# Kernel optimization log

Hardware: AMD Instinct MI355X
Metric: run time of the kernel (lower is better)

Reference implementation:

```python
import jax, jax.numpy as jnp
import numpy as np

B = 10      # number of interacting objects
NDIM = 2    # self.n: position/velocity dimensionality

# Edge list equivalent to rel_rec/rel_send one-hot matrices (edges grouped by receiver)
_rec_idx, _send_idx = np.where(~np.eye(B, dtype=bool))


def _mlp(x, W0, b0, W1, b1, W2, b2):
    # MLP with 2 hidden softplus layers, linear output
    h = jax.nn.softplus(x @ W0 + b0)
    h = jax.nn.softplus(h @ W1 + b1)
    return h @ W2 + b2


def setup_inputs() -> dict:
    key = jax.random.key(0)
    ks = jax.random.split(key, 7)
    N = 8192            # trajectories per batch
    H = 128             # hidden width of self-dynamics MLP
    Hi = 128            # hidden width of interaction MLP
    nin = 2 * NDIM      # self MLP input dim (pos+vel)
    nout = 2 * NDIM     # n_f_out for order=1
    nin_i = 3 * NDIM    # interaction MLP input dim (p1-p2, v1, v2)
    w = lambda k, shp: jax.random.normal(k, shp, jnp.float32) / np.float32(np.sqrt(shp[0]))
    return {
        "z": jax.random.normal(ks[0], (N * B, 2 * NDIM), jnp.float32),
        "fW0": w(ks[1], (nin, H)),   "fb0": jnp.zeros((H,), jnp.float32),
        "fW1": w(ks[2], (H, H)),     "fb1": jnp.zeros((H,), jnp.float32),
        "fW2": w(ks[3], (H, nout)),  "fb2": jnp.zeros((nout,), jnp.float32),
        "iW0": w(ks[4], (nin_i, Hi)),"ib0": jnp.zeros((Hi,), jnp.float32),
        "iW1": w(ks[5], (Hi, Hi)),   "ib1": jnp.zeros((Hi,), jnp.float32),
        "iW2": w(ks[6], (Hi, nout)), "ib2": jnp.zeros((nout,), jnp.float32),
    }


def reference(z, fW0, fb0, fW1, fb1, fW2, fb2, iW0, ib0, iW1, ib1, iW2, ib2):
    # One evaluation of the ODE vector field (order=1, n_aug_dyn=n_aug_st=0).
    n = NDIM
    NB = z.shape[0]
    N = NB // B
    dz_self = _mlp(z, fW0, fb0, fW1, fb1, fW2, fb2)            # [N*B, 2n]
    z3 = z.reshape(N, B, 2 * n)
    recv = z3[:, _rec_idx]                                     # [N, B(B-1), 2n] gather (node2edge)
    send = z3[:, _send_idx]
    # odefint input: (p_recv - p_send, v_recv, v_send)  -> [N, B(B-1), 3n]
    inp = jnp.concatenate([recv[..., :n] - send[..., :n], recv[..., n:], send[..., n:]], -1)
    dz_int = _mlp(inp, iW0, ib0, iW1, ib1, iW2, ib2)           # [N, B(B-1), 2n]
    dz_int = dz_int.reshape(N, B, B - 1, 2 * n).sum(2)         # sum over senders per receiver
    dz = dz_self.reshape(N, B, 2 * n) + dz_int
    return dz.reshape(NB, 2 * n)
```

## Files before the change

kernel.cpp:

```cpp
#include <hip/hip_runtime.h>
#include <hip/hip_bf16.h>

#define NDIM 2
#define BB 10
#define H 128
#define PAIRS 90
#define ROWS 112
#define LDH 136
#define LOG2E 1.4426950408889634f
#define LN2   0.6931471805599453f

typedef short short8 __attribute__((ext_vector_type(8)));
typedef float floatx4 __attribute__((ext_vector_type(4)));

__device__ inline short f2bf(float x) {
    unsigned u = __float_as_uint(x);
    return (short)((u + 0x7fffu + ((u >> 16) & 1u)) >> 16);
}

#if __has_builtin(__builtin_amdgcn_cvt_pk_bf16_f32)
typedef __bf16 bf16x2_t __attribute__((ext_vector_type(2)));
__device__ inline unsigned pk2(float a, float b) {
    bf16x2_t v = __builtin_amdgcn_cvt_pk_bf16_f32(a, b);
    return __builtin_bit_cast(unsigned, v);
}
#else
__device__ inline unsigned pk2(float a, float b) {
    unsigned ua = __float_as_uint(a), ub = __float_as_uint(b);
    ua = (ua + 0x7fffu + ((ua >> 16) & 1u)) >> 16;
    ub = (ub + 0x7fffu + ((ub >> 16) & 1u)) & 0xffff0000u;
    return ua | ub;
}
#endif

__device__ inline float sp2(float xs) {
#if __has_builtin(__builtin_amdgcn_exp2f) && __has_builtin(__builtin_amdgcn_logf)
    float t = __builtin_amdgcn_exp2f(xs);
    return __builtin_amdgcn_logf(1.f + t) * LN2;
#else
    return log2f(1.f + exp2f(xs)) * LN2;
#endif
}

__global__ void prep_weights(const float* __restrict__ iW1, const float* __restrict__ fW1,
                             const float* __restrict__ iW2, const float* __restrict__ fW2,
                             const float* __restrict__ ib1, const float* __restrict__ fb1,
                             short* __restrict__ W1Fi, short* __restrict__ W1Ff,
                             short* __restrict__ W2Fi, short* __restrict__ W2Ff,
                             float* __restrict__ ib1s, float* __restrict__ fb1s) {
    int t = blockIdx.x * blockDim.x + threadIdx.x;
    int stride = gridDim.x * blockDim.x;
    for (int fidx = t; fidx < 16384; fidx += stride) {
        int j = fidx & 7, lane = (fidx >> 3) & 63, nt = (fidx >> 9) & 7, ks = fidx >> 12;
        int k = 32 * ks + ((lane >> 4) << 3) + j;
        int n = 16 * nt + (lane & 15);
        W1Fi[fidx] = f2bf(iW1[k * H + n] * LOG2E);
        W1Ff[fidx] = f2bf(fW1[k * H + n] * LOG2E);
    }
    for (int fidx = t; fidx < 2048; fidx += stride) {
        int j = fidx & 7, lane = (fidx >> 3) & 63, ks = fidx >> 9;
        int k = 32 * ks + ((lane >> 4) << 3) + j;
        int n = lane & 15;
        W2Fi[fidx] = (n < 4) ? f2bf(iW2[k * 4 + n]) : (short)0;
        W2Ff[fidx] = (n < 4) ? f2bf(fW2[k * 4 + n]) : (short)0;
    }
    if (t < 128) {
        ib1s[t] = ib1[t] * LOG2E;
        fb1s[t] = fb1[t] * LOG2E;
    }
}

__global__ __launch_bounds__(512, 4) void fused_kernel(
    const float* __restrict__ z,
    const float* __restrict__ iW0, const float* __restrict__ ib0,
    const float* __restrict__ ib2,
    const float* __restrict__ fW0, const float* __restrict__ fb0,
    const float* __restrict__ fb2,
    const short* __restrict__ W1Fi, const short* __restrict__ W2Fi,
    const short* __restrict__ W1Ff, const short* __restrict__ W2Ff,
    const float* __restrict__ ib1s, const float* __restrict__ fb1s,
    float* __restrict__ out) {
    __shared__ __align__(16) short h0s[ROWS * LDH];
    __shared__ __align__(16) float uws[2560];
    __shared__ __align__(16) float4 zs4[BB];
    float* us   = uws;
    float* wss  = uws + 1280;
    float* outs = uws;

    int n = blockIdx.x;
    int tid = threadIdx.x, lane = tid & 63, wave = tid >> 6;
    int rit = lane & 15, quad = lane >> 4;
    int nt = wave;

    short8 w1[4], fa[4];
#pragma unroll
    for (int ks = 0; ks < 4; ++ks) {
        w1[ks] = *(const short8*)(W1Fi + ((ks * 8 + nt) * 64 + lane) * 8);
        fa[ks] = *(const short8*)(W1Ff + ((ks * 8 + nt) * 64 + lane) * 8);
    }

    if (tid < BB) zs4[tid] = ((const float4*)z)[n * BB + tid];
    __syncthreads();

    {
        int c = tid & 127;
        float iw0 = iW0[c] * LOG2E, iw1 = iW0[128 + c] * LOG2E;
        float iw2 = iW0[256 + c] * LOG2E, iw3 = iW0[384 + c] * LOG2E;
        float iw4 = iW0[512 + c] * LOG2E, iw5 = iW0[640 + c] * LOG2E;
        float ib = ib0[c] * LOG2E;
        int b0 = tid >> 7;
#pragma unroll
        for (int t = 0; t < 3; ++t) {
            int b = b0 + 4 * t;
            if (b < BB) {
                float4 zb = zs4[b];
                us[b * 128 + c]  = ib + zb.x * iw0 + zb.y * iw1 + zb.z * iw2 + zb.w * iw3;
                wss[b * 128 + c] = -zb.x * iw0 - zb.y * iw1 + zb.z * iw4 + zb.w * iw5;
            }
        }
    }
#pragma unroll
    for (int t = 0; t < 2; ++t) {
        int u = tid + 512 * t;
        if (u < 640) {
            int b = u >> 6, c2 = (u & 63) * 2;
            float4 zb = zs4[b];
            float2 w0 = *(const float2*)(fW0 + c2);
            float2 w1_ = *(const float2*)(fW0 + 128 + c2);
            float2 w2_ = *(const float2*)(fW0 + 256 + c2);
            float2 w3 = *(const float2*)(fW0 + 384 + c2);
            float2 bb = *(const float2*)(fb0 + c2);
            float a0 = bb.x + zb.x * w0.x + zb.y * w1_.x + zb.z * w2_.x + zb.w * w3.x;
            float a1 = bb.y + zb.x * w0.y + zb.y * w1_.y + zb.z * w2_.y + zb.w * w3.y;
            *(unsigned*)(h0s + (96 + b) * LDH + c2) = pk2(sp2(a0 * LOG2E), sp2(a1 * LOG2E));
        }
    }
    if (tid < 192) {
        int r = 106 + (tid >> 5), kk = (tid & 31) * 4;
        *(uint2*)(h0s + r * LDH + kk) = uint2{0u, 0u};
    }
    __syncthreads();

    {
        int kk = (tid & 31) << 2;
        int m0 = tid >> 5;
#pragma unroll
        for (int t = 0; t < 6; ++t) {
            int m = m0 + 16 * t;
            uint2 pk = {0u, 0u};
            if (m < PAIRS) {
                int i = (m * 57) >> 9;
                int s = m - 9 * i;
                int j = s + (s >= i);
                float4 uu = *(float4*)(us + i * 128 + kk);
                float4 ww = *(float4*)(wss + j * 128 + kk);
                pk.x = pk2(sp2(uu.x + ww.x), sp2(uu.y + ww.y));
                pk.y = pk2(sp2(uu.z + ww.z), sp2(uu.w + ww.w));
            }
            *(uint2*)(h0s + m * LDH + kk) = pk;
        }
    }
    __syncthreads();

    float4 bi = *(const float4*)(ib1s + 16 * nt + 4 * quad);
    float4 bs = *(const float4*)(fb1s + 16 * nt + 4 * quad);
    floatx4 acc[7];
#pragma unroll
    for (int mt = 0; mt < 6; ++mt) acc[mt] = floatx4{bi.x, bi.y, bi.z, bi.w};
    acc[6] = floatx4{bs.x, bs.y, bs.z, bs.w};
#pragma unroll
    for (int ks = 0; ks < 4; ++ks) {
        short8 bf[7];
#pragma unroll
        for (int mt = 0; mt < 7; ++mt)
            bf[mt] = *(const short8*)(h0s + (16 * mt + rit) * LDH + 32 * ks + quad * 8);
#pragma unroll
        for (int mt = 0; mt < 6; ++mt)
            acc[mt] = __builtin_amdgcn_mfma_f32_16x16x32_bf16(w1[ks], bf[mt], acc[mt], 0, 0, 0);
        acc[6] = __builtin_amdgcn_mfma_f32_16x16x32_bf16(fa[ks], bf[6], acc[6], 0, 0, 0);
    }
    __syncthreads();

#pragma unroll
    for (int mt = 0; mt < 7; ++mt) {
        floatx4 a = acc[mt];
        uint2 pk;
        pk.x = pk2(sp2(a[0]), sp2(a[1]));
        pk.y = pk2(sp2(a[2]), sp2(a[3]));
        *(uint2*)(h0s + (16 * mt + rit) * LDH + 16 * nt + 4 * quad) = pk;
    }
    __syncthreads();

    if (wave < 7) {
        const short* W2 = (wave == 6) ? W2Ff : W2Fi;
        const float* b2 = (wave == 6) ? fb2 : ib2;
        short8 w2[4];
#pragma unroll
        for (int ks = 0; ks < 4; ++ks)
            w2[ks] = *(const short8*)(W2 + (ks * 64 + lane) * 8);
        floatx4 a = {0.f, 0.f, 0.f, 0.f};
        if (quad == 0) {
            float4 bb = *(const float4*)b2;
            a = floatx4{bb.x, bb.y, bb.z, bb.w};
        }
#pragma unroll
        for (int ks = 0; ks < 4; ++ks) {
            short8 bf = *(const short8*)(h0s + (16 * wave + rit) * LDH + 32 * ks + quad * 8);
            a = __builtin_amdgcn_mfma_f32_16x16x32_bf16(w2[ks], bf, a, 0, 0, 0);
        }
        if (quad == 0) {
            float4 o = {a[0], a[1], a[2], a[3]};
            *(float4*)(outs + (16 * wave + rit) * 4) = o;
        }
    }
    __syncthreads();

    if (tid < BB * 4) {
        int i = tid >> 2, c = tid & 3;
        float s = outs[(96 + i) * 4 + c];
#pragma unroll
        for (int p = 0; p < 9; ++p) s += outs[(9 * i + p) * 4 + c];
        out[(n * BB + i) * 4 + c] = s;
    }
}

extern "C" void kernel_launch(void* const* d_in, const int* in_sizes, int n_in,
                              void* d_out, int out_size, void* d_ws, size_t ws_size,
                              hipStream_t stream) {
    const float* z   = (const float*)d_in[0];
    const float* fW0 = (const float*)d_in[1];
    const float* fb0 = (const float*)d_in[2];
    const float* fW1 = (const float*)d_in[3];
    const float* fb1 = (const float*)d_in[4];
    const float* fW2 = (const float*)d_in[5];
    const float* fb2 = (const float*)d_in[6];
    const float* iW0 = (const float*)d_in[7];
    const float* ib0 = (const float*)d_in[8];
    const float* iW1 = (const float*)d_in[9];
    const float* ib1 = (const float*)d_in[10];
    const float* iW2 = (const float*)d_in[11];
    const float* ib2 = (const float*)d_in[12];
    float* out = (float*)d_out;

    short* wsS = (short*)d_ws;
    short* W1Fi = wsS;
    short* W1Ff = wsS + 16384;
    short* W2Fi = wsS + 32768;
    short* W2Ff = wsS + 34816;
    float* ib1s = (float*)(wsS + 36864);
    float* fb1s = ib1s + 128;

    int NB = in_sizes[0] / (2 * NDIM);
    int Nsys = NB / BB;

    hipLaunchKernelGGL(prep_weights, dim3(64), dim3(256), 0, stream,
                       iW1, fW1, iW2, fW2, ib1, fb1,
                       W1Fi, W1Ff, W2Fi, W2Ff, ib1s, fb1s);
    hipLaunchKernelGGL(fused_kernel, dim3(Nsys), dim3(512), 0, stream,
                       z, iW0, ib0, ib2, fW0, fb0, fb2,
                       W1Fi, W2Fi, W1Ff, W2Ff, ib1s, fb1s, out);
}
```

Baseline: 190.7 us.

## Switch layer-1 GEMM to 32x32x16 MFMA with reworked wave tiling

Rewrites the hidden-layer GEMM to use 32x32x16 bf16 MFMA tiles. Each wave now covers a 32-column slice and two 32-row blocks, and the self-MLP weight fragments are reloaded for the upper row block. Layer-0 weights and biases are pre-scaled by log2e in the prep kernel, the first-layer fills are widened to 128-bit stores, and the u/w scratch is padded to reduce bank conflicts. Launch bounds are raised to 6 blocks per CU, which risks register pressure from the 16-wide accumulators and the 8 retained A fragments.

```diff
diff --git a/kernel.cpp b/kernel.cpp
--- a/kernel.cpp
+++ b/kernel.cpp
@@ -5,13 +5,14 @@
 #define BB 10
 #define H 128
 #define PAIRS 90
-#define ROWS 112
+#define MROWS 128
 #define LDH 136
+#define USLD 132
 #define LOG2E 1.4426950408889634f
-#define LN2   0.6931471805599453f
 
 typedef short short8 __attribute__((ext_vector_type(8)));
 typedef float floatx4 __attribute__((ext_vector_type(4)));
+typedef float floatx16 __attribute__((ext_vector_type(16)));
 
 __device__ inline short f2bf(float x) {
     unsigned u = __float_as_uint(x);
@@ -36,24 +37,26 @@
 __device__ inline float sp2(float xs) {
 #if __has_builtin(__builtin_amdgcn_exp2f) && __has_builtin(__builtin_amdgcn_logf)
     float t = __builtin_amdgcn_exp2f(xs);
-    return __builtin_amdgcn_logf(1.f + t) * LN2;
+    return __builtin_amdgcn_logf(1.f + t) * 0.6931471805599453f;
 #else
-    return log2f(1.f + exp2f(xs)) * LN2;
+    return log2f(1.f + exp2f(xs)) * 0.6931471805599453f;
 #endif
 }
 
 __global__ void prep_weights(const float* __restrict__ iW1, const float* __restrict__ fW1,
                              const float* __restrict__ iW2, const float* __restrict__ fW2,
                              const float* __restrict__ ib1, const float* __restrict__ fb1,
+                             const float* __restrict__ iW0, const float* __restrict__ ib0,
+                             const float* __restrict__ fW0, const float* __restrict__ fb0,
                              short* __restrict__ W1Fi, short* __restrict__ W1Ff,
                              short* __restrict__ W2Fi, short* __restrict__ W2Ff,
-                             float* __restrict__ ib1s, float* __restrict__ fb1s) {
+                             float* __restrict__ scal) {
     int t = blockIdx.x * blockDim.x + threadIdx.x;
     int stride = gridDim.x * blockDim.x;
     for (int fidx = t; fidx < 16384; fidx += stride) {
-        int j = fidx & 7, lane = (fidx >> 3) & 63, nt = (fidx >> 9) & 7, ks = fidx >> 12;
-        int k = 32 * ks + ((lane >> 4) << 3) + j;
-        int n = 16 * nt + (lane & 15);
+        int j = fidx & 7, lane = (fidx >> 3) & 63, nt = (fidx >> 9) & 3, ks = fidx >> 11;
+        int k = 16 * ks + ((lane >> 5) << 3) + j;
+        int n = 32 * nt + (lane & 31);
         W1Fi[fidx] = f2bf(iW1[k * H + n] * LOG2E);
         W1Ff[fidx] = f2bf(fW1[k * H + n] * LOG2E);
     }
@@ -65,152 +68,175 @@
         W2Ff[fidx] = (n < 4) ? f2bf(fW2[k * 4 + n]) : (short)0;
     }
     if (t < 128) {
-        ib1s[t] = ib1[t] * LOG2E;
-        fb1s[t] = fb1[t] * LOG2E;
-    }
-}
-
-__global__ __launch_bounds__(512, 4) void fused_kernel(
+        scal[t] = ib1[t] * LOG2E;
+        scal[128 + t] = fb1[t] * LOG2E;
+        scal[1024 + t] = ib0[t] * LOG2E;
+        scal[1664 + t] = fb0[t] * LOG2E;
+    }
+    if (t < 768) scal[256 + t] = iW0[t] * LOG2E;
+    if (t < 512) scal[1152 + t] = fW0[t] * LOG2E;
+}
+
+__global__ __launch_bounds__(512, 6) void fused_kernel(
     const float* __restrict__ z,
-    const float* __restrict__ iW0, const float* __restrict__ ib0,
-    const float* __restrict__ ib2,
-    const float* __restrict__ fW0, const float* __restrict__ fb0,
-    const float* __restrict__ fb2,
+    const float* __restrict__ ib2, const float* __restrict__ fb2,
     const short* __restrict__ W1Fi, const short* __restrict__ W2Fi,
     const short* __restrict__ W1Ff, const short* __restrict__ W2Ff,
-    const float* __restrict__ ib1s, const float* __restrict__ fb1s,
-    float* __restrict__ out) {
-    __shared__ __align__(16) short h0s[ROWS * LDH];
-    __shared__ __align__(16) float uws[2560];
+    const float* __restrict__ scal, float* __restrict__ out) {
+    __shared__ __align__(16) short h0s[MROWS * LDH];
+    __shared__ __align__(16) float uws[2 * BB * USLD];
     __shared__ __align__(16) float4 zs4[BB];
     float* us   = uws;
-    float* wss  = uws + 1280;
+    float* wss  = uws + BB * USLD;
     float* outs = uws;
 
     int n = blockIdx.x;
     int tid = threadIdx.x, lane = tid & 63, wave = tid >> 6;
-    int rit = lane & 15, quad = lane >> 4;
-    int nt = wave;
-
-    short8 w1[4], fa[4];
-#pragma unroll
-    for (int ks = 0; ks < 4; ++ks) {
-        w1[ks] = *(const short8*)(W1Fi + ((ks * 8 + nt) * 64 + lane) * 8);
-        fa[ks] = *(const short8*)(W1Ff + ((ks * 8 + nt) * 64 + lane) * 8);
-    }
+    int c31 = lane & 31, halfk = lane >> 5;
+    int ntw = wave & 3, mhalf = wave >> 2;
+
+    short8 af[8];
+#pragma unroll
+    for (int ks = 0; ks < 8; ++ks)
+        af[ks] = *(const short8*)(W1Fi + ((ks * 4 + ntw) * 64 + lane) * 8);
 
     if (tid < BB) zs4[tid] = ((const float4*)z)[n * BB + tid];
     __syncthreads();
 
     {
         int c = tid & 127;
-        float iw0 = iW0[c] * LOG2E, iw1 = iW0[128 + c] * LOG2E;
-        float iw2 = iW0[256 + c] * LOG2E, iw3 = iW0[384 + c] * LOG2E;
-        float iw4 = iW0[512 + c] * LOG2E, iw5 = iW0[640 + c] * LOG2E;
-        float ib = ib0[c] * LOG2E;
-        int b0 = tid >> 7;
+        const float* iW0s = scal + 256;
+        float w0 = iW0s[c], w1 = iW0s[128 + c], w2 = iW0s[256 + c];
+        float w3 = iW0s[384 + c], w4 = iW0s[512 + c], w5 = iW0s[640 + c];
+        float b0v = scal[1024 + c];
+        int bb0 = tid >> 7;
 #pragma unroll
         for (int t = 0; t < 3; ++t) {
-            int b = b0 + 4 * t;
+            int b = bb0 + 4 * t;
             if (b < BB) {
                 float4 zb = zs4[b];
-                us[b * 128 + c]  = ib + zb.x * iw0 + zb.y * iw1 + zb.z * iw2 + zb.w * iw3;
-                wss[b * 128 + c] = -zb.x * iw0 - zb.y * iw1 + zb.z * iw4 + zb.w * iw5;
-            }
-        }
-    }
-#pragma unroll
-    for (int t = 0; t < 2; ++t) {
-        int u = tid + 512 * t;
-        if (u < 640) {
-            int b = u >> 6, c2 = (u & 63) * 2;
-            float4 zb = zs4[b];
-            float2 w0 = *(const float2*)(fW0 + c2);
-            float2 w1_ = *(const float2*)(fW0 + 128 + c2);
-            float2 w2_ = *(const float2*)(fW0 + 256 + c2);
-            float2 w3 = *(const float2*)(fW0 + 384 + c2);
-            float2 bb = *(const float2*)(fb0 + c2);
-            float a0 = bb.x + zb.x * w0.x + zb.y * w1_.x + zb.z * w2_.x + zb.w * w3.x;
-            float a1 = bb.y + zb.x * w0.y + zb.y * w1_.y + zb.z * w2_.y + zb.w * w3.y;
-            *(unsigned*)(h0s + (96 + b) * LDH + c2) = pk2(sp2(a0 * LOG2E), sp2(a1 * LOG2E));
-        }
-    }
-    if (tid < 192) {
-        int r = 106 + (tid >> 5), kk = (tid & 31) * 4;
-        *(uint2*)(h0s + r * LDH + kk) = uint2{0u, 0u};
-    }
-    __syncthreads();
-
-    {
-        int kk = (tid & 31) << 2;
-        int m0 = tid >> 5;
-#pragma unroll
-        for (int t = 0; t < 6; ++t) {
-            int m = m0 + 16 * t;
-            uint2 pk = {0u, 0u};
+                us[b * USLD + c]  = b0v + zb.x * w0 + zb.y * w1 + zb.z * w2 + zb.w * w3;
+                wss[b * USLD + c] = -zb.x * w0 - zb.y * w1 + zb.z * w4 + zb.w * w5;
+            }
+        }
+    }
+    if (tid < 320) {
+        int b = tid >> 5, c4 = (tid & 31) * 4;
+        const float* fW0s = scal + 1152;
+        float4 zb = zs4[b];
+        float4 q0 = *(const float4*)(fW0s + c4);
+        float4 q1 = *(const float4*)(fW0s + 128 + c4);
+        float4 q2 = *(const float4*)(fW0s + 256 + c4);
+        float4 q3 = *(const float4*)(fW0s + 384 + c4);
+        float4 qb = *(const float4*)(scal + 1664 + c4);
+        float a0 = qb.x + zb.x * q0.x + zb.y * q1.x + zb.z * q2.x + zb.w * q3.x;
+        float a1 = qb.y + zb.x * q0.y + zb.y * q1.y + zb.z * q2.y + zb.w * q3.y;
+        float a2 = qb.z + zb.x * q0.z + zb.y * q1.z + zb.z * q2.z + zb.w * q3.z;
+        float a3 = qb.w + zb.x * q0.w + zb.y * q1.w + zb.z * q2.w + zb.w * q3.w;
+        uint2 pk;
+        pk.x = pk2(sp2(a0), sp2(a1));
+        pk.y = pk2(sp2(a2), sp2(a3));
+        *(uint2*)(h0s + (96 + b) * LDH + c4) = pk;
+    }
+    if (tid < 352) {
+        int r = 106 + (tid >> 4), kk8 = (tid & 15) * 8;
+        *(uint4*)(h0s + r * LDH + kk8) = uint4{0u, 0u, 0u, 0u};
+    }
+    __syncthreads();
+
+    {
+        int m0 = tid >> 4, kk8 = (tid & 15) * 8;
+#pragma unroll
+        for (int t = 0; t < 3; ++t) {
+            int m = m0 + 32 * t;
+            uint4 pk = {0u, 0u, 0u, 0u};
             if (m < PAIRS) {
                 int i = (m * 57) >> 9;
                 int s = m - 9 * i;
                 int j = s + (s >= i);
-                float4 uu = *(float4*)(us + i * 128 + kk);
-                float4 ww = *(float4*)(wss + j * 128 + kk);
-                pk.x = pk2(sp2(uu.x + ww.x), sp2(uu.y + ww.y));
-                pk.y = pk2(sp2(uu.z + ww.z), sp2(uu.w + ww.w));
-            }
-            *(uint2*)(h0s + m * LDH + kk) = pk;
-        }
-    }
-    __syncthreads();
-
-    float4 bi = *(const float4*)(ib1s + 16 * nt + 4 * quad);
-    float4 bs = *(const float4*)(fb1s + 16 * nt + 4 * quad);
-    floatx4 acc[7];
-#pragma unroll
-    for (int mt = 0; mt < 6; ++mt) acc[mt] = floatx4{bi.x, bi.y, bi.z, bi.w};
-    acc[6] = floatx4{bs.x, bs.y, bs.z, bs.w};
-#pragma unroll
-    for (int ks = 0; ks < 4; ++ks) {
-        short8 bf[7];
-#pragma unroll
-        for (int mt = 0; mt < 7; ++mt)
-            bf[mt] = *(const short8*)(h0s + (16 * mt + rit) * LDH + 32 * ks + quad * 8);
-#pragma unroll
-        for (int mt = 0; mt < 6; ++mt)
-            acc[mt] = __builtin_amdgcn_mfma_f32_16x16x32_bf16(w1[ks], bf[mt], acc[mt], 0, 0, 0);
-        acc[6] = __builtin_amdgcn_mfma_f32_16x16x32_bf16(fa[ks], bf[6], acc[6], 0, 0, 0);
-    }
-    __syncthreads();
-
-#pragma unroll
-    for (int mt = 0; mt < 7; ++mt) {
-        floatx4 a = acc[mt];
-        uint2 pk;
-        pk.x = pk2(sp2(a[0]), sp2(a[1]));
-        pk.y = pk2(sp2(a[2]), sp2(a[3]));
-        *(uint2*)(h0s + (16 * mt + rit) * LDH + 16 * nt + 4 * quad) = pk;
-    }
-    __syncthreads();
-
-    if (wave < 7) {
-        const short* W2 = (wave == 6) ? W2Ff : W2Fi;
-        const float* b2 = (wave == 6) ? fb2 : ib2;
-        short8 w2[4];
-#pragma unroll
-        for (int ks = 0; ks < 4; ++ks)
-            w2[ks] = *(const short8*)(W2 + (ks * 64 + lane) * 8);
-        floatx4 a = {0.f, 0.f, 0.f, 0.f};
-        if (quad == 0) {
-            float4 bb = *(const float4*)b2;
-            a = floatx4{bb.x, bb.y, bb.z, bb.w};
-        }
-#pragma unroll
-        for (int ks = 0; ks < 4; ++ks) {
-            short8 bf = *(const short8*)(h0s + (16 * wave + rit) * LDH + 32 * ks + quad * 8);
-            a = __builtin_amdgcn_mfma_f32_16x16x32_bf16(w2[ks], bf, a, 0, 0, 0);
-        }
-        if (quad == 0) {
-            float4 o = {a[0], a[1], a[2], a[3]};
-            *(float4*)(outs + (16 * wave + rit) * 4) = o;
+                float4 ua = *(float4*)(us + i * USLD + kk8);
+                float4 ub = *(float4*)(us + i * USLD + kk8 + 4);
+                float4 wa = *(float4*)(wss + j * USLD + kk8);
+                float4 wb = *(float4*)(wss + j * USLD + kk8 + 4);
+                pk.x = pk2(sp2(ua.x + wa.x), sp2(ua.y + wa.y));
+                pk.y = pk2(sp2(ua.z + wa.z), sp2(ua.w + wa.w));
+                pk.z = pk2(sp2(ub.x + wb.x), sp2(ub.y + wb.y));
+                pk.w = pk2(sp2(ub.z + wb.z), sp2(ub.w + wb.w));
+            }
+            *(uint4*)(h0s + m * LDH + kk8) = pk;
+        }
+    }
+    __syncthreads();
+
+    int hb = 32 * ntw + 4 * halfk;
+    floatx16 acc0, acc1;
+    {
+        const float* blo = scal;
+        const float* bhi = mhalf ? (scal + 128) : scal;
+#pragma unroll
+        for (int g = 0; g < 4; ++g) {
+            float4 v0 = *(const float4*)(blo + hb + 8 * g);
+            float4 v1 = *(const float4*)(bhi + hb + 8 * g);
+            acc0[4 * g + 0] = v0.x; acc0[4 * g + 1] = v0.y;
+            acc0[4 * g + 2] = v0.z; acc0[4 * g + 3] = v0.w;
+            acc1[4 * g + 0] = v1.x; acc1[4 * g + 1] = v1.y;
+            acc1[4 * g + 2] = v1.z; acc1[4 * g + 3] = v1.w;
+        }
+    }
+    int rowA = 64 * mhalf + c31;
+    int rowB = rowA + 32;
+#pragma unroll
+    for (int ks = 0; ks < 8; ++ks) {
+        short8 bf = *(const short8*)(h0s + rowA * LDH + 16 * ks + 8 * halfk);
+        acc0 = __builtin_amdgcn_mfma_f32_32x32x16_bf16(af[ks], bf, acc0, 0, 0, 0);
+    }
+    if (mhalf) {
+#pragma unroll
+        for (int ks = 0; ks < 8; ++ks)
+            af[ks] = *(const short8*)(W1Ff + ((ks * 4 + ntw) * 64 + lane) * 8);
+    }
+#pragma unroll
+    for (int ks = 0; ks < 8; ++ks) {
+        short8 bf = *(const short8*)(h0s + rowB * LDH + 16 * ks + 8 * halfk);
+        acc1 = __builtin_amdgcn_mfma_f32_32x32x16_bf16(af[ks], bf, acc1, 0, 0, 0);
+    }
+    __syncthreads();
+
+#pragma unroll
+    for (int g = 0; g < 4; ++g) {
+        uint2 pa, pb;
+        pa.x = pk2(sp2(acc0[4 * g + 0]), sp2(acc0[4 * g + 1]));
+        pa.y = pk2(sp2(acc0[4 * g + 2]), sp2(acc0[4 * g + 3]));
+        pb.x = pk2(sp2(acc1[4 * g + 0]), sp2(acc1[4 * g + 1]));
+        pb.y = pk2(sp2(acc1[4 * g + 2]), sp2(acc1[4 * g + 3]));
+        *(uint2*)(h0s + rowA * LDH + 32 * ntw + 8 * g + 4 * halfk) = pa;
+        *(uint2*)(h0s + rowB * LDH + 32 * ntw + 8 * g + 4 * halfk) = pb;
+    }
+    __syncthreads();
+
+    {
+        int rit = lane & 15, quad = lane >> 4;
+        if (wave < 7) {
+            const short* W2 = (wave == 6) ? W2Ff : W2Fi;
+            const float* b2 = (wave == 6) ? fb2 : ib2;
+            short8 w2v[4];
+#pragma unroll
+            for (int ks = 0; ks < 4; ++ks)
+                w2v[ks] = *(const short8*)(W2 + (ks * 64 + lane) * 8);
+            floatx4 a = {0.f, 0.f, 0.f, 0.f};
+            if (quad == 0) {
+                float4 bbv = *(const float4*)b2;
+                a = floatx4{bbv.x, bbv.y, bbv.z, bbv.w};
+            }
+#pragma unroll
+            for (int ks = 0; ks < 4; ++ks) {
+                short8 bf = *(const short8*)(h0s + (16 * wave + rit) * LDH + 32 * ks + quad * 8);
+                a = __builtin_amdgcn_mfma_f32_16x16x32_bf16(w2v[ks], bf, a, 0, 0, 0);
+            }
+            if (quad == 0) {
+                float4 o = {a[0], a[1], a[2], a[3]};
+                *(float4*)(outs + (16 * wave + rit) * 4) = o;
+            }
         }
     }
     __syncthreads();
@@ -247,16 +273,14 @@
     short* W1Ff = wsS + 16384;
     short* W2Fi = wsS + 32768;
     short* W2Ff = wsS + 34816;
-    float* ib1s = (float*)(wsS + 36864);
-    float* fb1s = ib1s + 128;
+    float* scal = (float*)(wsS + 36864);
 
     int NB = in_sizes[0] / (2 * NDIM);
     int Nsys = NB / BB;
 
-    hipLaunchKernelGGL(prep_weights, dim3(64), dim3(256), 0, stream,
-                       iW1, fW1, iW2, fW2, ib1, fb1,
-                       W1Fi, W1Ff, W2Fi, W2Ff, ib1s, fb1s);
+    hipLaunchKernelGGL(prep_weights, dim3(128), dim3(256), 0, stream,
+                       iW1, fW1, iW2, fW2, ib1, fb1, iW0, ib0, fW0, fb0,
+                       W1Fi, W1Ff, W2Fi, W2Ff, scal);
     hipLaunchKernelGGL(fused_kernel, dim3(Nsys), dim3(512), 0, stream,
-                       z, iW0, ib0, ib2, fW0, fb0, fb2,
-                       W1Fi, W2Fi, W1Ff, W2Ff, ib1s, fb1s, out);
-}
+                       z, ib2, fb2, W1Fi, W2Fi, W1Ff, W2Ff, scal, out);
+}
```

Measured after the change: 181.8 us. 1.05x faster.
